# Kernel tuning notes

Hardware: AMD Instinct MI355X
Metric: run time of the kernel (lower is better)

Reference implementation:

```python
import jax, jax.numpy as jnp
import numpy as np

DIMS = 1024; HEAD = 16; HD = DIMS // HEAD
MAX_DIST = 1024; MAX_SPAN = 1024; TEMP_SCALE = 0.01
SCALE = HD ** -0.25  # hd^-0.25 per the torch modules


def _layer_norm(x, g, b, eps=1e-5):
    m = jnp.mean(x, -1, keepdims=True)
    v = jnp.mean((x - m) ** 2, -1, keepdims=True)
    return (x - m) * jax.lax.rsqrt(v + eps) * g + b


def _forward(x, ln_a_g, ln_a_b, ln_b_g, ln_b_b, Wq, bq, Wk, Wv, bv, Wc, bc, Wp, bp, Wo, bo):
    B, S, D = x.shape
    local = _layer_norm(x, ln_a_g, ln_a_b)
    globe = _layer_norm(x, ln_b_g, ln_b_b)
    # --- global path: QueryModule/KeyModule/ValueModule + AttentionCombiner SDPA (mask=None) ---
    q = (globe @ Wq.T + bq).reshape(B, S, HEAD, HD).transpose(0, 2, 1, 3) * SCALE
    k = (globe @ Wk.T).reshape(B, S, HEAD, HD).transpose(0, 2, 1, 3) * SCALE
    v = (globe @ Wv.T + bv).reshape(B, S, HEAD, HD).transpose(0, 2, 1, 3)
    # SDPA applies its own 1/sqrt(hd) on top of the modules' hd^-0.25 scalings (faithful to torch)
    scores = jnp.einsum('bhqd,bhkd->bhqk', q, k) / jnp.sqrt(jnp.asarray(HD, x.dtype))
    w = jax.nn.softmax(scores, -1)
    g_out = jnp.einsum('bhqk,bhkd->bhqd', w, v).transpose(0, 2, 1, 3).reshape(B, S, D)
    g_out = g_out @ Wc.T + bc
    # --- span predictor; torch uses span_scale.mean().item() which detaches -> stop_gradient ---
    span_scale = jax.nn.sigmoid(jnp.mean(g_out, 1) @ Wp.T + bp)  # [B,1]
    span_mean = jax.lax.stop_gradient(jnp.mean(span_scale))
    span_len = jnp.minimum(jnp.floor(MAX_SPAN * span_mean).astype(jnp.int32), S)
    eff = jnp.maximum(jnp.minimum(span_len, MAX_DIST), 1)  # eff_span (>=1 to keep softmax finite)
    temp = 1.0 + TEMP_SCALE * (1.0 - span_mean)  # sharpen=True branch
    # --- local AdaptiveSpan path: q[:, :eff], k[:, :eff], v[:, :eff] expressed as masking
    #     so shapes stay static under jit; rows >= eff are the zero-padding of the span output.
    lh = local.reshape(B, S, HEAD, HD).transpose(0, 2, 1, 3)  # [B,H,S,hd]
    ls = jnp.einsum('bhqd,bhkd->bhqk', lh, lh) / temp * SCALE
    valid = jnp.arange(S) < eff
    ls = jnp.where(valid[None, None, None, :], ls, jnp.asarray(-1e30, x.dtype))
    lw = jax.nn.softmax(ls, -1)
    l_out = jnp.einsum('bhqk,bhkd->bhqd', lw, lh).transpose(0, 2, 1, 3).reshape(B, S, D)
    l_out = jnp.where(valid[None, :, None], l_out, jnp.asarray(0.0, x.dtype))
    combined = jnp.concatenate([l_out, g_out], -1)  # [B,S,2D]
    return combined @ Wo.T + bo


def setup_inputs() -> dict:
    key = jax.random.key(0)
    ks = jax.random.split(key, 8)
    B, S = 2, 1024
    nrm = lambda k, sh, std=0.02: jax.random.normal(k, sh, jnp.float32) * std
    return {
        'x': jax.random.normal(ks[0], (B, S, DIMS), jnp.float32),
        'ln_a_g': jnp.ones(DIMS, jnp.float32), 'ln_a_b': jnp.zeros(DIMS, jnp.float32),
        'ln_b_g': jnp.ones(DIMS, jnp.float32), 'ln_b_b': jnp.zeros(DIMS, jnp.float32),
        'Wq': nrm(ks[1], (DIMS, DIMS)), 'bq': jnp.zeros(DIMS, jnp.float32),
        'Wk': nrm(ks[2], (DIMS, DIMS)),
        'Wv': nrm(ks[3], (DIMS, DIMS)), 'bv': jnp.zeros(DIMS, jnp.float32),
        'Wc': nrm(ks[4], (DIMS, DIMS)), 'bc': jnp.zeros(DIMS, jnp.float32),
        'Wp': nrm(ks[5], (1, DIMS), (2.0 / (DIMS + 1)) ** 0.5), 'bp': jnp.zeros(1, jnp.float32),
        'Wo': nrm(ks[6], (DIMS, 2 * DIMS)), 'bo': jnp.zeros(DIMS, jnp.float32),
    }


def reference(x, ln_a_g, ln_a_b, ln_b_g, ln_b_b, Wq, bq, Wk, Wv, bv, Wc, bc, Wp, bp, Wo, bo):
    return _forward(x, ln_a_g, ln_a_b, ln_b_g, ln_b_b, Wq, bq, Wk, Wv, bv, Wc, bc, Wp, bp, Wo, bo)
```

## Files before the change

kernel.cpp:

```cpp
#include <hip/hip_runtime.h>
#include <math.h>

#define S_LEN 1024
#define DIMS  1024
#define NHEAD 16
#define HD    64
#define BATCH 2
#define MROWS (BATCH * S_LEN)
#define LOG2E 1.44269504088896f

typedef unsigned short us;
typedef __attribute__((ext_vector_type(8))) __bf16 bf8_t;
typedef __attribute__((ext_vector_type(8))) unsigned short us8_t;
typedef __attribute__((ext_vector_type(4))) unsigned short us4_t;
typedef __attribute__((ext_vector_type(4))) float f32x4;

static __device__ inline us f2bf(float f) {
    unsigned int u = __builtin_bit_cast(unsigned int, f);
    unsigned int r = u + 0x7fffu + ((u >> 16) & 1u);
    return (us)(r >> 16);
}
static __device__ inline float bf2f(us v) {
    unsigned int u = ((unsigned int)v) << 16;
    return __builtin_bit_cast(float, u);
}
static __device__ inline unsigned int pk2bf(float lo, float hi) {
    unsigned int r;
    asm("v_cvt_pk_bf16_f32 %0, %1, %2" : "=v"(r) : "v"(lo), "v"(hi));
    return r;
}
static __device__ inline f32x4 mfma16(us8_t a, us8_t b, f32x4 c) {
    return __builtin_amdgcn_mfma_f32_16x16x32_bf16(
        __builtin_bit_cast(bf8_t, a), __builtin_bit_cast(bf8_t, b), c, 0, 0, 0);
}

__global__ __launch_bounds__(256) void cvt5_kernel(
    const float* __restrict__ s0, const float* __restrict__ s1,
    const float* __restrict__ s2, const float* __restrict__ s3,
    const float* __restrict__ s4,
    us* __restrict__ d0, us* __restrict__ d1, us* __restrict__ d2,
    us* __restrict__ d3, us* __restrict__ d4)
{
    int bidx = blockIdx.x;
    const float* src; us* dst; int blk;
    if (bidx < 1024)      { src = s0; dst = d0; blk = bidx; }
    else if (bidx < 2048) { src = s1; dst = d1; blk = bidx - 1024; }
    else if (bidx < 3072) { src = s2; dst = d2; blk = bidx - 2048; }
    else if (bidx < 4096) { src = s3; dst = d3; blk = bidx - 3072; }
    else                  { src = s4; dst = d4; blk = bidx - 4096; }
    size_t idx = (size_t)blk * 1024 + threadIdx.x * 4;
    float4 v = *(const float4*)(src + idx);
    us4_t ot;
    ot[0] = f2bf(v.x); ot[1] = f2bf(v.y); ot[2] = f2bf(v.z); ot[3] = f2bf(v.w);
    *(us4_t*)(dst + idx) = ot;
}

__global__ __launch_bounds__(256) void ln2_kernel(
    const float* __restrict__ x,
    const float* __restrict__ ga, const float* __restrict__ ba,
    const float* __restrict__ gb, const float* __restrict__ bb,
    us* __restrict__ outA, us* __restrict__ outB)
{
    int row = blockIdx.x;
    int t = threadIdx.x;
    const float* xr = x + (size_t)row * DIMS;
    float4 v = *(const float4*)(xr + t * 4);
    float s  = v.x + v.y + v.z + v.w;
    float s2 = v.x * v.x + v.y * v.y + v.z * v.z + v.w * v.w;
#pragma unroll
    for (int o = 32; o > 0; o >>= 1) {
        s  += __shfl_down(s, o, 64);
        s2 += __shfl_down(s2, o, 64);
    }
    __shared__ float rs[4], rs2[4];
    int wid = t >> 6, lane = t & 63;
    if (lane == 0) { rs[wid] = s; rs2[wid] = s2; }
    __syncthreads();
    float S0 = rs[0] + rs[1] + rs[2] + rs[3];
    float S2 = rs2[0] + rs2[1] + rs2[2] + rs2[3];
    float mean = S0 * (1.0f / DIMS);
    float var  = S2 * (1.0f / DIMS) - mean * mean;
    float inv  = 1.0f / sqrtf(var + 1e-5f);
    float4 vga = *(const float4*)(ga + t * 4);
    float4 vba = *(const float4*)(ba + t * 4);
    float4 vgb = *(const float4*)(gb + t * 4);
    float4 vbb = *(const float4*)(bb + t * 4);
    float nx = (v.x - mean) * inv, ny = (v.y - mean) * inv;
    float nz = (v.z - mean) * inv, nw = (v.w - mean) * inv;
    us4_t oa, ob;
    oa[0] = f2bf(nx * vga.x + vba.x); oa[1] = f2bf(ny * vga.y + vba.y);
    oa[2] = f2bf(nz * vga.z + vba.z); oa[3] = f2bf(nw * vga.w + vba.w);
    ob[0] = f2bf(nx * vgb.x + vbb.x); ob[1] = f2bf(ny * vgb.y + vbb.y);
    ob[2] = f2bf(nz * vgb.z + vbb.z); ob[3] = f2bf(nw * vgb.w + vbb.w);
    *(us4_t*)(outA + (size_t)row * DIMS + t * 4) = oa;
    *(us4_t*)(outB + (size_t)row * DIMS + t * 4) = ob;
}

template <int OUTBF>
static __device__ __forceinline__ void gemm128_body(
    const us* __restrict__ A, int lda,
    const us* __restrict__ W, int ldw,
    const float* __restrict__ bias,
    void* __restrict__ Cp, int ldc, int K,
    int bm, int bn, us* As, us* Bs)
{
    int tid = threadIdx.x;
    int w = tid >> 6, l = tid & 63, l15 = l & 15, lhi = l >> 4;
    int wr = w >> 1, wc = w & 1;
    f32x4 acc[4][2];
#pragma unroll
    for (int m = 0; m < 4; ++m) { acc[m][0] = (f32x4){0,0,0,0}; acc[m][1] = (f32x4){0,0,0,0}; }
    int srow = tid >> 3;
    int scol8 = tid & 7;
    int sl = (scol8 ^ (srow & 7)) * 8;
    const us* Ap = A + (size_t)(bm + srow) * lda + scol8 * 8;
    const us* Wpt = W + (size_t)(bn + srow) * ldw + scol8 * 8;
    us8_t a0 = *(const us8_t*)(Ap);
    us8_t a1 = *(const us8_t*)(Ap + (size_t)32 * lda);
    us8_t a2 = *(const us8_t*)(Ap + (size_t)64 * lda);
    us8_t a3 = *(const us8_t*)(Ap + (size_t)96 * lda);
    us8_t b0 = *(const us8_t*)(Wpt);
    us8_t b1 = *(const us8_t*)(Wpt + (size_t)32 * ldw);
    int xorbase = l15 & 7;
    for (int kt = 0; kt < K; kt += 64) {
        __syncthreads();
        *(us8_t*)&As[(srow +  0) * 64 + sl] = a0;
        *(us8_t*)&As[(srow + 32) * 64 + sl] = a1;
        *(us8_t*)&As[(srow + 64) * 64 + sl] = a2;
        *(us8_t*)&As[(srow + 96) * 64 + sl] = a3;
        *(us8_t*)&Bs[(srow +  0) * 64 + sl] = b0;
        *(us8_t*)&Bs[(srow + 32) * 64 + sl] = b1;
        __syncthreads();
        if (kt + 64 < K) {
            a0 = *(const us8_t*)(Ap + kt + 64);
            a1 = *(const us8_t*)(Ap + (size_t)32 * lda + kt + 64);
            a2 = *(const us8_t*)(Ap + (size_t)64 * lda + kt + 64);
            a3 = *(const us8_t*)(Ap + (size_t)96 * lda + kt + 64);
            b0 = *(const us8_t*)(Wpt + kt + 64);
            b1 = *(const us8_t*)(Wpt + (size_t)32 * ldw + kt + 64);
        }
#pragma unroll
        for (int kk = 0; kk < 2; ++kk) {
            int xo = ((kk * 4 + lhi) ^ xorbase) * 8;
            us8_t af[4], bfr[2];
#pragma unroll
            for (int m = 0; m < 4; ++m)
                af[m] = *(const us8_t*)&As[(wr * 64 + m * 16 + l15) * 64 + xo];
#pragma unroll
            for (int n = 0; n < 2; ++n)
                bfr[n] = *(const us8_t*)&Bs[(wc * 32 + n * 16 + l15) * 64 + xo];
#pragma unroll
            for (int m = 0; m < 4; ++m)
#pragma unroll
                for (int n = 0; n < 2; ++n)
                    acc[m][n] = mfma16(af[m], bfr[n], acc[m][n]);
        }
    }
    float bvv[2] = {0.f, 0.f};
    if (bias) {
#pragma unroll
        for (int n = 0; n < 2; ++n)
            bvv[n] = bias[bn + wc * 32 + n * 16 + l15];
    }
#pragma unroll
    for (int m = 0; m < 4; ++m) {
#pragma unroll
        for (int n = 0; n < 2; ++n) {
            int row = bm + wr * 64 + m * 16 + lhi * 4;
            int col = bn + wc * 32 + n * 16 + l15;
            if (OUTBF) {
                us* Cb = (us*)Cp;
                unsigned int p01 = pk2bf(acc[m][n][0] + bvv[n], acc[m][n][1] + bvv[n]);
                unsigned int p23 = pk2bf(acc[m][n][2] + bvv[n], acc[m][n][3] + bvv[n]);
                Cb[(size_t)(row + 0) * ldc + col] = (us)p01;
                Cb[(size_t)(row + 1) * ldc + col] = (us)(p01 >> 16);
                Cb[(size_t)(row + 2) * ldc + col] = (us)p23;
                Cb[(size_t)(row + 3) * ldc + col] = (us)(p23 >> 16);
            } else {
                float* Cf = (float*)Cp;
#pragma unroll
                for (int r = 0; r < 4; ++r)
                    Cf[(size_t)(row + r) * ldc + col] = acc[m][n][r] + bvv[n];
            }
        }
    }
}

template <int OUTBF>
__global__ __launch_bounds__(256) void gemm128(
    const us* __restrict__ A, int lda,
    const us* __restrict__ W, int ldw,
    const float* __restrict__ bias,
    void* __restrict__ Cp, int ldc, int K)
{
    __shared__ __align__(16) us As[128 * 64];
    __shared__ __align__(16) us Bs[64 * 64];
    gemm128_body<OUTBF>(A, lda, W, ldw, bias, Cp, ldc, K,
                        blockIdx.y * 128, blockIdx.x * 64, As, Bs);
}

__global__ __launch_bounds__(256) void gemm_qkv(
    const us* __restrict__ A,
    const us* __restrict__ Wq, const us* __restrict__ Wk, const us* __restrict__ Wv,
    const float* __restrict__ bq, const float* __restrict__ bv,
    us* __restrict__ qo, us* __restrict__ ko, us* __restrict__ vo)
{
    __shared__ __align__(16) us As[128 * 64];
    __shared__ __align__(16) us Bs[64 * 64];
    int which = blockIdx.x >> 4;
    int bn = (blockIdx.x & 15) * 64, bm = blockIdx.y * 128;
    const us* W = (which == 0) ? Wq : ((which == 1) ? Wk : Wv);
    const float* bias = (which == 0) ? bq : ((which == 2) ? bv : nullptr);
    us* Out = (which == 0) ? qo : ((which == 1) ? ko : vo);
    gemm128_body<1>(A, DIMS, W, DIMS, bias, Out, DIMS, DIMS, bm, bn, As, Bs);
}

template <int OUTBF>
__global__ __launch_bounds__(256) void gemm_bf16(
    const us* __restrict__ A, int lda,
    const us* __restrict__ W, int ldw,
    const float* __restrict__ bias,
    void* __restrict__ Cp, int ldc, int K)
{
    __shared__ __align__(16) us As[64 * 64];
    __shared__ __align__(16) us Bs[64 * 64];
    int tid = threadIdx.x;
    int w = tid >> 6, l = tid & 63, l15 = l & 15, lhi = l >> 4;
    int wr = w >> 1, wc = w & 1;
    int bm = blockIdx.y * 64, bn = blockIdx.x * 64;
    f32x4 acc[2][2] = {{{0,0,0,0},{0,0,0,0}},{{0,0,0,0},{0,0,0,0}}};
    int srow = tid >> 3;
    int scol8 = tid & 7;
    const us* Ap = A + (size_t)(bm + srow) * lda + scol8 * 8;
    const us* Wpt = W + (size_t)(bn + srow) * ldw + scol8 * 8;
    int sl = (scol8 ^ (srow & 7)) * 8;
    us8_t a0 = *(const us8_t*)(Ap);
    us8_t a1 = *(const us8_t*)(Ap + (size_t)32 * lda);
    us8_t b0 = *(const us8_t*)(Wpt);
    us8_t b1 = *(const us8_t*)(Wpt + (size_t)32 * ldw);
    int xorbase = l15 & 7;
    for (int kt = 0; kt < K; kt += 64) {
        __syncthreads();
        *(us8_t*)&As[srow * 64 + sl] = a0;
        *(us8_t*)&As[(srow + 32) * 64 + sl] = a1;
        *(us8_t*)&Bs[srow * 64 + sl] = b0;
        *(us8_t*)&Bs[(srow + 32) * 64 + sl] = b1;
        __syncthreads();
        if (kt + 64 < K) {
            a0 = *(const us8_t*)(Ap + kt + 64);
            a1 = *(const us8_t*)(Ap + (size_t)32 * lda + kt + 64);
            b0 = *(const us8_t*)(Wpt + kt + 64);
            b1 = *(const us8_t*)(Wpt + (size_t)32 * ldw + kt + 64);
        }
#pragma unroll
        for (int kk = 0; kk < 2; ++kk) {
            int xo = ((kk * 4 + lhi) ^ xorbase) * 8;
            us8_t af[2], bfr[2];
#pragma unroll
            for (int m = 0; m < 2; ++m)
                af[m] = *(const us8_t*)&As[(wr * 32 + m * 16 + l15) * 64 + xo];
#pragma unroll
            for (int n = 0; n < 2; ++n)
                bfr[n] = *(const us8_t*)&Bs[(wc * 32 + n * 16 + l15) * 64 + xo];
#pragma unroll
            for (int m = 0; m < 2; ++m)
#pragma unroll
                for (int n = 0; n < 2; ++n)
                    acc[m][n] = mfma16(af[m], bfr[n], acc[m][n]);
        }
    }
    float bvv[2] = {0.f, 0.f};
    if (bias) {
#pragma unroll
        for (int n = 0; n < 2; ++n)
            bvv[n] = bias[bn + wc * 32 + n * 16 + l15];
    }
#pragma unroll
    for (int m = 0; m < 2; ++m) {
#pragma unroll
        for (int n = 0; n < 2; ++n) {
            int row = bm + wr * 32 + m * 16 + lhi * 4;
            int col = bn + wc * 32 + n * 16 + l15;
            if (OUTBF) {
                us* Cb = (us*)Cp;
                unsigned int p01 = pk2bf(acc[m][n][0] + bvv[n], acc[m][n][1] + bvv[n]);
                unsigned int p23 = pk2bf(acc[m][n][2] + bvv[n], acc[m][n][3] + bvv[n]);
                Cb[(size_t)(row + 0) * ldc + col] = (us)p01;
                Cb[(size_t)(row + 1) * ldc + col] = (us)(p01 >> 16);
                Cb[(size_t)(row + 2) * ldc + col] = (us)p23;
                Cb[(size_t)(row + 3) * ldc + col] = (us)(p23 >> 16);
            } else {
                float* Cf = (float*)Cp;
#pragma unroll
                for (int r = 0; r < 4; ++r)
                    Cf[(size_t)(row + r) * ldc + col] = acc[m][n][r] + bvv[n];
            }
        }
    }
}

template <int LOCAL>
__global__ __launch_bounds__(512) void attn_mfma(
    const us* __restrict__ Q, const us* __restrict__ K,
    const us* __restrict__ V, us* __restrict__ O, int ldo,
    const float* __restrict__ span)
{
    __shared__ __align__(16) us Ks[2][64 * 64];
    __shared__ __align__(16) us Vt[2][64 * 64];
    __shared__ __align__(16) us Ps[8][16 * 64];

    int b = blockIdx.z, h = blockIdx.y;
    int q0blk = blockIdx.x * 64;
    int tid = threadIdx.x;
    int w = tid >> 6, l = tid & 63;
    int l15 = l & 15, lhi = l >> 4;
    int wq = w & 3, wk = w >> 2;

    float scale; int eff;
    if (LOCAL) { scale = span[1] * LOG2E; eff = (int)span[0]; }
    else       { scale = LOG2E / 64.0f; eff = S_LEN; }
    int ntiles = LOCAL ? ((eff + 63) >> 6) : 16;
    int nIter = (ntiles + 1) >> 1;

    int qrow = q0blk + wq * 16 + l15;
    const us* qptr = Q + ((size_t)(b * S_LEN + qrow)) * DIMS + h * HD + lhi * 8;
    us8_t qf[2];
    qf[0] = *(const us8_t*)(qptr);
    qf[1] = *(const us8_t*)(qptr + 32);

    f32x4 o[4] = {{0,0,0,0},{0,0,0,0},{0,0,0,0},{0,0,0,0}};
    float m_r[4] = {-1e30f, -1e30f, -1e30f, -1e30f};
    float l_r[4] = {0.f, 0.f, 0.f, 0.f};

    int half = tid >> 8;
    int t0 = tid & 255;
    int krow = t0 >> 3, kcol8 = t0 & 7;
    int ksl = (kcol8 ^ (krow & 7)) * 8;
    int vkb = t0 & 15, vdb = t0 >> 4;
    const us* Kb = K + ((size_t)(b * S_LEN)) * DIMS + h * HD;
    const us* Vb = V + ((size_t)(b * S_LEN)) * DIMS + h * HD;

    us8_t kc0, kc1;
    us4_t vr0, vr1, vr2, vr3;
    if (half < ntiles) {
        const us* kp = Kb + (size_t)(half * 64 + krow) * DIMS + kcol8 * 8;
        kc0 = *(const us8_t*)kp;
        kc1 = *(const us8_t*)(kp + (size_t)32 * DIMS);
        const us* vp = Vb + (size_t)(half * 64 + vkb * 4) * DIMS + vdb * 4;
        vr0 = *(const us4_t*)(vp);
        vr1 = *(const us4_t*)(vp + DIMS);
        vr2 = *(const us4_t*)(vp + 2 * DIMS);
        vr3 = *(const us4_t*)(vp + 3 * DIMS);
    }

    for (int i = 0; i < nIter; ++i) {
        __syncthreads();
        if (2 * i + half < ntiles) {
            *(us8_t*)&Ks[half][krow * 64 + ksl] = kc0;
            *(us8_t*)&Ks[half][(krow + 32) * 64 + ksl] = kc1;
#pragma unroll
            for (int j = 0; j < 4; ++j) {
                int d = vdb * 4 + j;
                us4_t wv;
                wv[0] = vr0[j]; wv[1] = vr1[j]; wv[2] = vr2[j]; wv[3] = vr3[j];
                int slot = (vkb >> 1) ^ (d & 7);
                *(us4_t*)&Vt[half][d * 64 + slot * 8 + (vkb & 1) * 4] = wv;
            }
        }
        __syncthreads();
        int nt2 = 2 * (i + 1) + half;
        if (nt2 < ntiles) {
            const us* kp = Kb + (size_t)(nt2 * 64 + krow) * DIMS + kcol8 * 8;
            kc0 = *(const us8_t*)kp;
            kc1 = *(const us8_t*)(kp + (size_t)32 * DIMS);
            const us* vp = Vb + (size_t)(nt2 * 64 + vkb * 4) * DIMS + vdb * 4;
            vr0 = *(const us4_t*)(vp);
            vr1 = *(const us4_t*)(vp + DIMS);
            vr2 = *(const us4_t*)(vp + 2 * DIMS);
            vr3 = *(const us4_t*)(vp + 3 * DIMS);
        }
        int kt = 2 * i + wk;
        if (kt < ntiles) {
            f32x4 s4[4] = {{0,0,0,0},{0,0,0,0},{0,0,0,0},{0,0,0,0}};
            __builtin_amdgcn_s_setprio(1);
#pragma unroll
            for (int kk = 0; kk < 2; ++kk) {
                int xo = ((kk * 4 + lhi) ^ (l15 & 7)) * 8;
#pragma unroll
                for (int n = 0; n < 4; ++n) {
                    us8_t bk = *(const us8_t*)&Ks[wk][(n * 16 + l15) * 64 + xo];
                    s4[n] = mfma16(qf[kk], bk, s4[n]);
                }
            }
            __builtin_amdgcn_s_setprio(0);
#pragma unroll
            for (int n = 0; n < 4; ++n) {
                s4[n] *= scale;
                if (LOCAL) {
                    int key = kt * 64 + n * 16 + l15;
                    if (key >= eff) {
                        s4[n][0] = -1e30f; s4[n][1] = -1e30f;
                        s4[n][2] = -1e30f; s4[n][3] = -1e30f;
                    }
                }
            }
            float tm[4];
#pragma unroll
            for (int r = 0; r < 4; ++r)
                tm[r] = fmaxf(fmaxf(s4[0][r], s4[1][r]), fmaxf(s4[2][r], s4[3][r]));
#pragma unroll
            for (int msk = 1; msk <= 8; msk <<= 1) {
#pragma unroll
                for (int r = 0; r < 4; ++r)
                    tm[r] = fmaxf(tm[r], __shfl_xor(tm[r], msk, 64));
            }
            bool upd = (tm[0] > m_r[0] + 11.5f) || (tm[1] > m_r[1] + 11.5f) ||
                       (tm[2] > m_r[2] + 11.5f) || (tm[3] > m_r[3] + 11.5f);
            if (upd) {
                float fac[4];
#pragma unroll
                for (int r = 0; r < 4; ++r) {
                    float mn = fmaxf(m_r[r], tm[r]);
                    fac[r] = exp2f(m_r[r] - mn);
                    m_r[r] = mn;
                    l_r[r] *= fac[r];
                }
#pragma unroll
                for (int n = 0; n < 4; ++n) {
                    o[n][0] *= fac[0]; o[n][1] *= fac[1];
                    o[n][2] *= fac[2]; o[n][3] *= fac[3];
                }
            }
#pragma unroll
            for (int n = 0; n < 4; ++n) {
                int col = n * 16 + l15;
                int slotbase = col >> 3;
                float p0 = exp2f(s4[n][0] - m_r[0]);
                float p1 = exp2f(s4[n][1] - m_r[1]);
                float p2 = exp2f(s4[n][2] - m_r[2]);
                float p3 = exp2f(s4[n][3] - m_r[3]);
                l_r[0] += p0; l_r[1] += p1; l_r[2] += p2; l_r[3] += p3;
                unsigned int p01 = pk2bf(p0, p1);
                unsigned int p23 = pk2bf(p2, p3);
                int q0 = lhi * 4;
                Ps[w][(q0 + 0) * 64 + ((slotbase ^ ((q0 + 0) & 7)) * 8) + (col & 7)] = (us)p01;
                Ps[w][(q0 + 1) * 64 + ((slotbase ^ ((q0 + 1) & 7)) * 8) + (col & 7)] = (us)(p01 >> 16);
                Ps[w][(q0 + 2) * 64 + ((slotbase ^ ((q0 + 2) & 7)) * 8) + (col & 7)] = (us)p23;
                Ps[w][(q0 + 3) * 64 + ((slotbase ^ ((q0 + 3) & 7)) * 8) + (col & 7)] = (us)(p23 >> 16);
            }
            __builtin_amdgcn_s_setprio(1);
#pragma unroll
            for (int kk = 0; kk < 2; ++kk) {
                int xo = ((kk * 4 + lhi) ^ (l15 & 7)) * 8;
                us8_t pa = *(const us8_t*)&Ps[w][l15 * 64 + ((kk * 4 + lhi) ^ (l15 & 7)) * 8];
#pragma unroll
                for (int n = 0; n < 4; ++n) {
                    us8_t vb = *(const us8_t*)&Vt[wk][(n * 16 + l15) * 64 + xo];
                    o[n] = mfma16(pa, vb, o[n]);
                }
            }
            __builtin_amdgcn_s_setprio(0);
        }
    }

#pragma unroll
    for (int msk = 1; msk <= 8; msk <<= 1) {
#pragma unroll
        for (int r = 0; r < 4; ++r)
            l_r[r] += __shfl_xor(l_r[r], msk, 64);
    }

    __syncthreads();
    float* obuf = (float*)&Ks[0][0];
    float* mlb  = (float*)&Vt[0][0];
    if (wk == 1) {
#pragma unroll
        for (int n = 0; n < 4; ++n)
#pragma unroll
            for (int r = 0; r < 4; ++r)
                obuf[wq * 1024 + (lhi * 4 + r) * 64 + n * 16 + l15] = o[n][r];
        if (l15 == 0) {
#pragma unroll
            for (int r = 0; r < 4; ++r) {
                mlb[wq * 32 + (lhi * 4 + r) * 2 + 0] = m_r[r];
                mlb[wq * 32 + (lhi * 4 + r) * 2 + 1] = l_r[r];
            }
        }
    }
    __syncthreads();
    if (wk == 0) {
        float f0[4], f1[4], rcp[4];
#pragma unroll
        for (int r = 0; r < 4; ++r) {
            int row = lhi * 4 + r;
            float m1 = mlb[wq * 32 + row * 2 + 0];
            float l1 = mlb[wq * 32 + row * 2 + 1];
            float ms = fmaxf(m_r[r], m1);
            f0[r] = exp2f(m_r[r] - ms);
            f1[r] = exp2f(m1 - ms);
            rcp[r] = 1.0f / (l_r[r] * f0[r] + l1 * f1[r]);
        }
#pragma unroll
        for (int n = 0; n < 4; ++n) {
            float vv[4];
#pragma unroll
            for (int r = 0; r < 4; ++r) {
                int row = q0blk + wq * 16 + lhi * 4 + r;
                float val = (o[n][r] * f0[r] +
                             obuf[wq * 1024 + (lhi * 4 + r) * 64 + n * 16 + l15] * f1[r]) * rcp[r];
                if (LOCAL && row >= eff) val = 0.0f;
                vv[r] = val;
            }
            int row0 = q0blk + wq * 16 + lhi * 4;
            unsigned int p01 = pk2bf(vv[0], vv[1]);
            unsigned int p23 = pk2bf(vv[2], vv[3]);
            size_t base = ((size_t)(b * S_LEN + row0)) * ldo + h * HD + n * 16 + l15;
            O[base + 0 * ldo] = (us)p01;
            O[base + 1 * ldo] = (us)(p01 >> 16);
            O[base + 2 * ldo] = (us)p23;
            O[base + 3 * ldo] = (us)(p23 >> 16);
        }
    }
}

__global__ __launch_bounds__(256) void span1_kernel(
    const us* __restrict__ gout, const float* __restrict__ Wp,
    float* __restrict__ partials)
{
    int slice = blockIdx.x;
    int b = blockIdx.y;
    int t = threadIdx.x;
    float4 wp = *(const float4*)(Wp + t * 4);
    float acc = 0;
    int s0 = slice * 128;
    for (int s = s0; s < s0 + 128; ++s) {
        us4_t g = *(const us4_t*)(gout + (size_t)(b * S_LEN + s) * 2048 + t * 4);
        acc += bf2f(g[0]) * wp.x + bf2f(g[1]) * wp.y + bf2f(g[2]) * wp.z + bf2f(g[3]) * wp.w;
    }
#pragma unroll
    for (int o = 32; o > 0; o >>= 1) acc += __shfl_down(acc, o, 64);
    __shared__ float r[4];
    int wid = t >> 6, lane = t & 63;
    if (lane == 0) r[wid] = acc;
    __syncthreads();
    if (t == 0) partials[b * 8 + slice] = r[0] + r[1] + r[2] + r[3];
}

__global__ void span2_kernel(const float* __restrict__ partials,
                             const float* __restrict__ bp,
                             float* __restrict__ spanbuf)
{
    if (threadIdx.x == 0 && blockIdx.x == 0) {
        float l0 = 0, l1 = 0;
        for (int i = 0; i < 8; ++i) { l0 += partials[i]; l1 += partials[8 + i]; }
        l0 = l0 * (1.0f / 1024.0f) + bp[0];
        l1 = l1 * (1.0f / 1024.0f) + bp[0];
        float s0 = 1.0f / (1.0f + expf(-l0));
        float s1 = 1.0f / (1.0f + expf(-l1));
        float sm = 0.5f * (s0 + s1);
        int sl = (int)floorf(1024.0f * sm);
        int eff = sl; if (eff > 1024) eff = 1024; if (eff < 1) eff = 1;
        float temp = 1.0f + 0.01f * (1.0f - sm);
        spanbuf[0] = (float)eff;
        spanbuf[1] = 0.35355339059327378f / temp;
    }
}

extern "C" void kernel_launch(void* const* d_in, const int* in_sizes, int n_in,
                              void* d_out, int out_size, void* d_ws, size_t ws_size,
                              hipStream_t stream)
{
    (void)in_sizes; (void)n_in; (void)out_size; (void)ws_size;
    const float* x   = (const float*)d_in[0];
    const float* lag = (const float*)d_in[1];
    const float* lab = (const float*)d_in[2];
    const float* lbg = (const float*)d_in[3];
    const float* lbb = (const float*)d_in[4];
    const float* Wq  = (const float*)d_in[5];
    const float* bq  = (const float*)d_in[6];
    const float* Wk  = (const float*)d_in[7];
    const float* Wv  = (const float*)d_in[8];
    const float* bv  = (const float*)d_in[9];
    const float* Wc  = (const float*)d_in[10];
    const float* bc  = (const float*)d_in[11];
    const float* Wp  = (const float*)d_in[12];
    const float* bp  = (const float*)d_in[13];
    const float* Wo  = (const float*)d_in[14];
    const float* bo  = (const float*)d_in[15];
    float* out = (float*)d_out;
    us* wsu = (us*)d_ws;

    const size_t NM = (size_t)MROWS * DIMS;
    us* lnAbf = wsu;
    us* lnBbf = wsu + NM;
    us* gattbf = lnBbf;
    us* qbf   = wsu + 2 * NM;
    us* kbf   = wsu + 3 * NM;
    us* vbf   = wsu + 4 * NM;
    us* combbf = qbf;
    us* Wqbf  = wsu + 5 * NM;
    us* Wkbf  = Wqbf + DIMS * DIMS;
    us* Wvbf  = Wkbf + DIMS * DIMS;
    us* Wcbf  = Wvbf + DIMS * DIMS;
    us* Wobf  = Wcbf + DIMS * DIMS;
    float* partials = (float*)(Wobf + 2 * DIMS * DIMS);
    float* spanbuf  = partials + 16;

    cvt5_kernel<<<6144, 256, 0, stream>>>(Wq, Wk, Wv, Wc, Wo,
                                          Wqbf, Wkbf, Wvbf, Wcbf, Wobf);

    ln2_kernel<<<MROWS, 256, 0, stream>>>(x, lag, lab, lbg, lbb, lnAbf, lnBbf);

    gemm_qkv<<<dim3(48, MROWS / 128), 256, 0, stream>>>(
        lnBbf, Wqbf, Wkbf, Wvbf, bq, bv, qbf, kbf, vbf);

    dim3 ag(S_LEN / 64, NHEAD, BATCH);
    attn_mfma<0><<<ag, 512, 0, stream>>>(qbf, kbf, vbf, gattbf, DIMS, nullptr);

    gemm_bf16<1><<<dim3(DIMS / 64, MROWS / 64), 256, 0, stream>>>(
        gattbf, DIMS, Wcbf, DIMS, bc, combbf + 1024, 2048, DIMS);

    span1_kernel<<<dim3(8, BATCH), 256, 0, stream>>>(combbf + 1024, Wp, partials);
    span2_kernel<<<1, 64, 0, stream>>>(partials, bp, spanbuf);

    attn_mfma<1><<<ag, 512, 0, stream>>>(lnAbf, lnAbf, lnAbf, combbf, 2048, spanbuf);

    gemm128<0><<<dim3(DIMS / 64, MROWS / 128), 256, 0, stream>>>(
        combbf, 2048, Wobf, 2048, bo, out, DIMS, 2 * DIMS);
}
```

Measured before the change: 143.7 us.

## Fuse prep and span kernels, remap attention grid per XCD, use transposed LDS reads

Merges the weight-conversion and dual layer-norm kernels into one launch, and folds the two span kernels into one using an atomic completion counter. The attention grid becomes a flat 512-block launch remapped so each (batch, head) pair stays on one XCD for K/V cache reuse. The P tile is now written in a layout that ds_read_b64_tr_b16 can read back as MFMA operands, and the max-rescale shuffle runs only when some lane actually needs an update. The output projection switches from the 128-row GEMM to the 64x64 tile GEMM. Together these trim launch overhead and LDS traffic, at the cost of inline asm and a counter that has to be reset on every call.

```diff
diff --git a/kernel.cpp b/kernel.cpp
--- a/kernel.cpp
+++ b/kernel.cpp
@@ -14,6 +14,7 @@
 typedef __attribute__((ext_vector_type(8))) unsigned short us8_t;
 typedef __attribute__((ext_vector_type(4))) unsigned short us4_t;
 typedef __attribute__((ext_vector_type(4))) float f32x4;
+typedef __attribute__((ext_vector_type(4))) unsigned int u32x4;
 
 static __device__ inline us f2bf(float f) {
     unsigned int u = __builtin_bit_cast(unsigned int, f);
@@ -34,52 +35,53 @@
         __builtin_bit_cast(bf8_t, a), __builtin_bit_cast(bf8_t, b), c, 0, 0, 0);
 }
 
-__global__ __launch_bounds__(256) void cvt5_kernel(
+__global__ __launch_bounds__(256) void prep_kernel(
     const float* __restrict__ s0, const float* __restrict__ s1,
     const float* __restrict__ s2, const float* __restrict__ s3,
     const float* __restrict__ s4,
     us* __restrict__ d0, us* __restrict__ d1, us* __restrict__ d2,
-    us* __restrict__ d3, us* __restrict__ d4)
-{
-    int bidx = blockIdx.x;
-    const float* src; us* dst; int blk;
-    if (bidx < 1024)      { src = s0; dst = d0; blk = bidx; }
-    else if (bidx < 2048) { src = s1; dst = d1; blk = bidx - 1024; }
-    else if (bidx < 3072) { src = s2; dst = d2; blk = bidx - 2048; }
-    else if (bidx < 4096) { src = s3; dst = d3; blk = bidx - 3072; }
-    else                  { src = s4; dst = d4; blk = bidx - 4096; }
-    size_t idx = (size_t)blk * 1024 + threadIdx.x * 4;
-    float4 v = *(const float4*)(src + idx);
-    us4_t ot;
-    ot[0] = f2bf(v.x); ot[1] = f2bf(v.y); ot[2] = f2bf(v.z); ot[3] = f2bf(v.w);
-    *(us4_t*)(dst + idx) = ot;
-}
-
-__global__ __launch_bounds__(256) void ln2_kernel(
+    us* __restrict__ d3, us* __restrict__ d4,
     const float* __restrict__ x,
     const float* __restrict__ ga, const float* __restrict__ ba,
     const float* __restrict__ gb, const float* __restrict__ bb,
-    us* __restrict__ outA, us* __restrict__ outB)
+    us* __restrict__ outA, us* __restrict__ outB,
+    unsigned int* __restrict__ ctr)
 {
-    int row = blockIdx.x;
+    int bidx = blockIdx.x;
     int t = threadIdx.x;
+    if (bidx == 0 && t == 0) *ctr = 0u;
+    if (bidx < 6144) {
+        const float* src; us* dst; int blk;
+        if (bidx < 1024)      { src = s0; dst = d0; blk = bidx; }
+        else if (bidx < 2048) { src = s1; dst = d1; blk = bidx - 1024; }
+        else if (bidx < 3072) { src = s2; dst = d2; blk = bidx - 2048; }
+        else if (bidx < 4096) { src = s3; dst = d3; blk = bidx - 3072; }
+        else                  { src = s4; dst = d4; blk = bidx - 4096; }
+        size_t idx = (size_t)blk * 1024 + t * 4;
+        float4 v = *(const float4*)(src + idx);
+        us4_t ot;
+        ot[0] = f2bf(v.x); ot[1] = f2bf(v.y); ot[2] = f2bf(v.z); ot[3] = f2bf(v.w);
+        *(us4_t*)(dst + idx) = ot;
+        return;
+    }
+    int row = bidx - 6144;
     const float* xr = x + (size_t)row * DIMS;
     float4 v = *(const float4*)(xr + t * 4);
-    float s  = v.x + v.y + v.z + v.w;
-    float s2 = v.x * v.x + v.y * v.y + v.z * v.z + v.w * v.w;
+    float sum1 = v.x + v.y + v.z + v.w;
+    float sumq = v.x * v.x + v.y * v.y + v.z * v.z + v.w * v.w;
 #pragma unroll
     for (int o = 32; o > 0; o >>= 1) {
-        s  += __shfl_down(s, o, 64);
-        s2 += __shfl_down(s2, o, 64);
-    }
-    __shared__ float rs[4], rs2[4];
+        sum1 += __shfl_down(sum1, o, 64);
+        sumq += __shfl_down(sumq, o, 64);
+    }
+    __shared__ float rs[4], rq[4];
     int wid = t >> 6, lane = t & 63;
-    if (lane == 0) { rs[wid] = s; rs2[wid] = s2; }
+    if (lane == 0) { rs[wid] = sum1; rq[wid] = sumq; }
     __syncthreads();
-    float S0 = rs[0] + rs[1] + rs[2] + rs[3];
-    float S2 = rs2[0] + rs2[1] + rs2[2] + rs2[3];
-    float mean = S0 * (1.0f / DIMS);
-    float var  = S2 * (1.0f / DIMS) - mean * mean;
+    float T1 = rs[0] + rs[1] + rs[2] + rs[3];
+    float T2 = rq[0] + rq[1] + rq[2] + rq[3];
+    float mean = T1 * (1.0f / DIMS);
+    float var  = T2 * (1.0f / DIMS) - mean * mean;
     float inv  = 1.0f / sqrtf(var + 1e-5f);
     float4 vga = *(const float4*)(ga + t * 4);
     float4 vba = *(const float4*)(ba + t * 4);
@@ -186,19 +188,6 @@
     }
 }
 
-template <int OUTBF>
-__global__ __launch_bounds__(256) void gemm128(
-    const us* __restrict__ A, int lda,
-    const us* __restrict__ W, int ldw,
-    const float* __restrict__ bias,
-    void* __restrict__ Cp, int ldc, int K)
-{
-    __shared__ __align__(16) us As[128 * 64];
-    __shared__ __align__(16) us Bs[64 * 64];
-    gemm128_body<OUTBF>(A, lda, W, ldw, bias, Cp, ldc, K,
-                        blockIdx.y * 128, blockIdx.x * 64, As, Bs);
-}
-
 __global__ __launch_bounds__(256) void gemm_qkv(
     const us* __restrict__ A,
     const us* __restrict__ Wq, const us* __restrict__ Wk, const us* __restrict__ Wv,
@@ -210,9 +199,9 @@
     int which = blockIdx.x >> 4;
     int bn = (blockIdx.x & 15) * 64, bm = blockIdx.y * 128;
     const us* W = (which == 0) ? Wq : ((which == 1) ? Wk : Wv);
-    const float* bias = (which == 0) ? bq : ((which == 2) ? bv : nullptr);
+    const float* bias2 = (which == 0) ? bq : ((which == 2) ? bv : nullptr);
     us* Out = (which == 0) ? qo : ((which == 1) ? ko : vo);
-    gemm128_body<1>(A, DIMS, W, DIMS, bias, Out, DIMS, DIMS, bm, bn, As, Bs);
+    gemm128_body<1>(A, DIMS, W, DIMS, bias2, Out, DIMS, DIMS, bm, bn, As, Bs);
 }
 
 template <int OUTBF>
@@ -307,10 +296,14 @@
 {
     __shared__ __align__(16) us Ks[2][64 * 64];
     __shared__ __align__(16) us Vt[2][64 * 64];
-    __shared__ __align__(16) us Ps[8][16 * 64];
-
-    int b = blockIdx.z, h = blockIdx.y;
-    int q0blk = blockIdx.x * 64;
+    __shared__ __align__(16) us Ps[8][1024];
+
+    int bid = blockIdx.x;
+    int xcd = bid & 7, slot = bid >> 3;
+    int p = xcd + 8 * (slot >> 4);
+    int q0blk = (slot & 15) * 64;
+    int h = p & 15, b = p >> 4;
+
     int tid = threadIdx.x;
     int w = tid >> 6, l = tid & 63;
     int l15 = l & 15, lhi = l >> 4;
@@ -339,6 +332,9 @@
     int vkb = t0 & 15, vdb = t0 >> 4;
     const us* Kb = K + ((size_t)(b * S_LEN)) * DIMS + h * HD;
     const us* Vb = V + ((size_t)(b * S_LEN)) * DIMS + h * HD;
+
+    unsigned pbase = (unsigned)(unsigned long long)&Ps[w][0];
+    unsigned paddr = pbase + (unsigned)(l * 8);
 
     us8_t kc0, kc1;
     us4_t vr0, vr1, vr2, vr3;
@@ -363,8 +359,8 @@
                 int d = vdb * 4 + j;
                 us4_t wv;
                 wv[0] = vr0[j]; wv[1] = vr1[j]; wv[2] = vr2[j]; wv[3] = vr3[j];
-                int slot = (vkb >> 1) ^ (d & 7);
-                *(us4_t*)&Vt[half][d * 64 + slot * 8 + (vkb & 1) * 4] = wv;
+                int slotv = (vkb >> 1) ^ (d & 7);
+                *(us4_t*)&Vt[half][d * 64 + slotv * 8 + (vkb & 1) * 4] = wv;
             }
         }
         __syncthreads();
@@ -404,23 +400,23 @@
                     }
                 }
             }
-            float tm[4];
+            float tl[4];
 #pragma unroll
             for (int r = 0; r < 4; ++r)
-                tm[r] = fmaxf(fmaxf(s4[0][r], s4[1][r]), fmaxf(s4[2][r], s4[3][r]));
-#pragma unroll
-            for (int msk = 1; msk <= 8; msk <<= 1) {
-#pragma unroll
-                for (int r = 0; r < 4; ++r)
-                    tm[r] = fmaxf(tm[r], __shfl_xor(tm[r], msk, 64));
-            }
-            bool upd = (tm[0] > m_r[0] + 11.5f) || (tm[1] > m_r[1] + 11.5f) ||
-                       (tm[2] > m_r[2] + 11.5f) || (tm[3] > m_r[3] + 11.5f);
-            if (upd) {
+                tl[r] = fmaxf(fmaxf(s4[0][r], s4[1][r]), fmaxf(s4[2][r], s4[3][r]));
+            int ex = (tl[0] > m_r[0] + 11.5f) | (tl[1] > m_r[1] + 11.5f) |
+                     (tl[2] > m_r[2] + 11.5f) | (tl[3] > m_r[3] + 11.5f);
+            if (__any(ex)) {
+#pragma unroll
+                for (int msk = 1; msk <= 8; msk <<= 1) {
+#pragma unroll
+                    for (int r = 0; r < 4; ++r)
+                        tl[r] = fmaxf(tl[r], __shfl_xor(tl[r], msk, 64));
+                }
                 float fac[4];
 #pragma unroll
                 for (int r = 0; r < 4; ++r) {
-                    float mn = fmaxf(m_r[r], tm[r]);
+                    float mn = fmaxf(m_r[r], tl[r]);
                     fac[r] = exp2f(m_r[r] - mn);
                     m_r[r] = mn;
                     l_r[r] *= fac[r];
@@ -433,8 +429,6 @@
             }
 #pragma unroll
             for (int n = 0; n < 4; ++n) {
-                int col = n * 16 + l15;
-                int slotbase = col >> 3;
                 float p0 = exp2f(s4[n][0] - m_r[0]);
                 float p1 = exp2f(s4[n][1] - m_r[1]);
                 float p2 = exp2f(s4[n][2] - m_r[2]);
@@ -442,17 +436,32 @@
                 l_r[0] += p0; l_r[1] += p1; l_r[2] += p2; l_r[3] += p3;
                 unsigned int p01 = pk2bf(p0, p1);
                 unsigned int p23 = pk2bf(p2, p3);
-                int q0 = lhi * 4;
-                Ps[w][(q0 + 0) * 64 + ((slotbase ^ ((q0 + 0) & 7)) * 8) + (col & 7)] = (us)p01;
-                Ps[w][(q0 + 1) * 64 + ((slotbase ^ ((q0 + 1) & 7)) * 8) + (col & 7)] = (us)(p01 >> 16);
-                Ps[w][(q0 + 2) * 64 + ((slotbase ^ ((q0 + 2) & 7)) * 8) + (col & 7)] = (us)p23;
-                Ps[w][(q0 + 3) * 64 + ((slotbase ^ ((q0 + 3) & 7)) * 8) + (col & 7)] = (us)(p23 >> 16);
-            }
+                int idx = (n >> 1) * 512 + ((l15 & 4) ? 256 : 0)
+                        + ((n & 1) * 2 + (l15 >> 3)) * 64 + (l15 & 3) * 16 + lhi * 4;
+                *(uint2*)&Ps[w][idx] = make_uint2(p01, p23);
+            }
+            unsigned long long ta0, ta1, ta2, ta3;
+            asm volatile(
+                "ds_read_b64_tr_b16 %0, %4\n\t"
+                "ds_read_b64_tr_b16 %1, %4 offset:512\n\t"
+                "ds_read_b64_tr_b16 %2, %4 offset:1024\n\t"
+                "ds_read_b64_tr_b16 %3, %4 offset:1536\n\t"
+                "s_waitcnt lgkmcnt(0)"
+                : "=&v"(ta0), "=&v"(ta1), "=&v"(ta2), "=&v"(ta3)
+                : "v"(paddr)
+                : "memory");
+            __builtin_amdgcn_sched_barrier(0);
+            u32x4 w0 = {(unsigned)ta0, (unsigned)(ta0 >> 32),
+                        (unsigned)ta1, (unsigned)(ta1 >> 32)};
+            u32x4 w1 = {(unsigned)ta2, (unsigned)(ta2 >> 32),
+                        (unsigned)ta3, (unsigned)(ta3 >> 32)};
+            us8_t pa0 = __builtin_bit_cast(us8_t, w0);
+            us8_t pa1 = __builtin_bit_cast(us8_t, w1);
             __builtin_amdgcn_s_setprio(1);
 #pragma unroll
             for (int kk = 0; kk < 2; ++kk) {
                 int xo = ((kk * 4 + lhi) ^ (l15 & 7)) * 8;
-                us8_t pa = *(const us8_t*)&Ps[w][l15 * 64 + ((kk * 4 + lhi) ^ (l15 & 7)) * 8];
+                us8_t pa = kk ? pa1 : pa0;
 #pragma unroll
                 for (int n = 0; n < 4; ++n) {
                     us8_t vb = *(const us8_t*)&Vt[wk][(n * 16 + l15) * 64 + xo];
@@ -523,17 +532,19 @@
     }
 }
 
-__global__ __launch_bounds__(256) void span1_kernel(
+__global__ __launch_bounds__(256) void span_fused(
     const us* __restrict__ gout, const float* __restrict__ Wp,
-    float* __restrict__ partials)
+    const float* __restrict__ bp,
+    float* __restrict__ partials, float* __restrict__ spanbuf,
+    unsigned int* __restrict__ ctr)
 {
     int slice = blockIdx.x;
     int b = blockIdx.y;
     int t = threadIdx.x;
     float4 wp = *(const float4*)(Wp + t * 4);
     float acc = 0;
-    int s0 = slice * 128;
-    for (int s = s0; s < s0 + 128; ++s) {
+    int srow0 = slice * 128;
+    for (int s = srow0; s < srow0 + 128; ++s) {
         us4_t g = *(const us4_t*)(gout + (size_t)(b * S_LEN + s) * 2048 + t * 4);
         acc += bf2f(g[0]) * wp.x + bf2f(g[1]) * wp.y + bf2f(g[2]) * wp.z + bf2f(g[3]) * wp.w;
     }
@@ -543,26 +554,25 @@
     int wid = t >> 6, lane = t & 63;
     if (lane == 0) r[wid] = acc;
     __syncthreads();
-    if (t == 0) partials[b * 8 + slice] = r[0] + r[1] + r[2] + r[3];
-}
-
-__global__ void span2_kernel(const float* __restrict__ partials,
-                             const float* __restrict__ bp,
-                             float* __restrict__ spanbuf)
-{
-    if (threadIdx.x == 0 && blockIdx.x == 0) {
-        float l0 = 0, l1 = 0;
-        for (int i = 0; i < 8; ++i) { l0 += partials[i]; l1 += partials[8 + i]; }
-        l0 = l0 * (1.0f / 1024.0f) + bp[0];
-        l1 = l1 * (1.0f / 1024.0f) + bp[0];
-        float s0 = 1.0f / (1.0f + expf(-l0));
-        float s1 = 1.0f / (1.0f + expf(-l1));
-        float sm = 0.5f * (s0 + s1);
-        int sl = (int)floorf(1024.0f * sm);
-        int eff = sl; if (eff > 1024) eff = 1024; if (eff < 1) eff = 1;
-        float temp = 1.0f + 0.01f * (1.0f - sm);
-        spanbuf[0] = (float)eff;
-        spanbuf[1] = 0.35355339059327378f / temp;
+    if (t == 0) {
+        partials[b * 8 + slice] = r[0] + r[1] + r[2] + r[3];
+        __threadfence();
+        unsigned int old = atomicAdd(ctr, 1u);
+        if (old == 15u) {
+            __threadfence();
+            float l0 = 0, l1 = 0;
+            for (int i = 0; i < 8; ++i) { l0 += partials[i]; l1 += partials[8 + i]; }
+            l0 = l0 * (1.0f / 1024.0f) + bp[0];
+            l1 = l1 * (1.0f / 1024.0f) + bp[0];
+            float sg0 = 1.0f / (1.0f + expf(-l0));
+            float sg1 = 1.0f / (1.0f + expf(-l1));
+            float sm = 0.5f * (sg0 + sg1);
+            int sl = (int)floorf(1024.0f * sm);
+            int eff = sl; if (eff > 1024) eff = 1024; if (eff < 1) eff = 1;
+            float temp = 1.0f + 0.01f * (1.0f - sm);
+            spanbuf[0] = (float)eff;
+            spanbuf[1] = 0.35355339059327378f / temp;
+        }
     }
 }
 
@@ -605,26 +615,26 @@
     us* Wobf  = Wcbf + DIMS * DIMS;
     float* partials = (float*)(Wobf + 2 * DIMS * DIMS);
     float* spanbuf  = partials + 16;
-
-    cvt5_kernel<<<6144, 256, 0, stream>>>(Wq, Wk, Wv, Wc, Wo,
-                                          Wqbf, Wkbf, Wvbf, Wcbf, Wobf);
-
-    ln2_kernel<<<MROWS, 256, 0, stream>>>(x, lag, lab, lbg, lbb, lnAbf, lnBbf);
+    unsigned int* spanctr = (unsigned int*)(spanbuf + 8);
+
+    prep_kernel<<<8192, 256, 0, stream>>>(Wq, Wk, Wv, Wc, Wo,
+                                          Wqbf, Wkbf, Wvbf, Wcbf, Wobf,
+                                          x, lag, lab, lbg, lbb, lnAbf, lnBbf,
+                                          spanctr);
 
     gemm_qkv<<<dim3(48, MROWS / 128), 256, 0, stream>>>(
         lnBbf, Wqbf, Wkbf, Wvbf, bq, bv, qbf, kbf, vbf);
 
-    dim3 ag(S_LEN / 64, NHEAD, BATCH);
-    attn_mfma<0><<<ag, 512, 0, stream>>>(qbf, kbf, vbf, gattbf, DIMS, nullptr);
+    attn_mfma<0><<<512, 512, 0, stream>>>(qbf, kbf, vbf, gattbf, DIMS, nullptr);
 
     gemm_bf16<1><<<dim3(DIMS / 64, MROWS / 64), 256, 0, stream>>>(
         gattbf, DIMS, Wcbf, DIMS, bc, combbf + 1024, 2048, DIMS);
 
-    span1_kernel<<<dim3(8, BATCH), 256, 0, stream>>>(combbf + 1024, Wp, partials);
-    span2_kernel<<<1, 64, 0, stream>>>(partials, bp, spanbuf);
-
-    attn_mfma<1><<<ag, 512, 0, stream>>>(lnAbf, lnAbf, lnAbf, combbf, 2048, spanbuf);
-
-    gemm128<0><<<dim3(DIMS / 64, MROWS / 128), 256, 0, stream>>>(
+    span_fused<<<dim3(8, BATCH), 256, 0, stream>>>(combbf + 1024, Wp, bp,
+                                                   partials, spanbuf, spanctr);
+
+    attn_mfma<1><<<512, 512, 0, stream>>>(lnAbf, lnAbf, lnAbf, combbf, 2048, spanbuf);
+
+    gemm_bf16<0><<<dim3(DIMS / 64, MROWS / 64), 256, 0, stream>>>(
         combbf, 2048, Wobf, 2048, bo, out, DIMS, 2 * DIMS);
 }
```

Result: faster. 126.6 us (-11.9%).
